# Optimization experiments

Measured on AMD Instinct MI355X. Metric: run time of the kernel, lower is better.

The kernel has to match this reference:

```python
import jax, jax.numpy as jnp
import numpy as np

BETA = 0.25  # commitment_beta


def setup_inputs() -> dict:
    key = jax.random.key(0)
    k1, k2 = jax.random.split(key)
    x = jax.random.normal(k1, (8, 256, 32, 32), dtype=jnp.float32)
    # nn.Embedding weight, uniform(-1/K, 1/K) in the original; use small randn-scaled init
    K, d = 4096, 256
    embed_w = jax.random.uniform(k2, (K, d), dtype=jnp.float32, minval=-1.0 / K, maxval=1.0 / K)
    return {"x": x, "embed_w": embed_w}


def reference(x, embed_w):
    B, C, H, W = x.shape
    N = H * W
    # b c h w -> b (h w) c
    xr = jnp.transpose(x, (0, 2, 3, 1)).reshape(B, N, C)
    flat = xr.reshape(B * N, C)
    dist = (-jnp.sum(flat * flat, axis=1, keepdims=True)
            - jnp.sum(embed_w * embed_w, axis=1)
            + 2.0 * jnp.einsum('nd,kd->nk', flat, embed_w))
    # temp=0.0 -> gumbel_sample degenerates to argmax
    embed_ind = jnp.argmax(dist, axis=-1).reshape(B, N)
    x_q = embed_w[embed_ind]  # [B, N, C] gather
    sg = jax.lax.stop_gradient
    loss = (BETA * jnp.mean((sg(x_q) - xr) ** 2)
            + jnp.mean((x_q - sg(xr)) ** 2))
    # straight-through estimator
    x_q = xr + sg(x_q - xr)
    # b (h w) c -> b c h w
    x_q = jnp.transpose(x_q.reshape(B, H, W, C), (0, 3, 1, 2))
    embed_ind = embed_ind.reshape(B, H, W)
    return (x_q, loss, embed_ind)
```

## Files before the change

### kernel.cpp

```cpp
#include <hip/hip_runtime.h>
#include <stdint.h>


typedef _Float16 f16;
typedef f16 half8 __attribute__((ext_vector_type(8)));
typedef float f32x4 __attribute__((ext_vector_type(4)));

__device__ __forceinline__ unsigned int sortable_f32(float v) {
    unsigned int u = __float_as_uint(v);
    return (u & 0x80000000u) ? ~u : (u | 0x80000000u);
}

__device__ __forceinline__ void gload_lds16(const void* g, void* l) {
    __builtin_amdgcn_global_load_lds(
        (const __attribute__((address_space(1))) unsigned int*)g,
        (__attribute__((address_space(3))) unsigned int*)l, 16, 0, 0);
}

__global__ void vq_prep(const float* __restrict__ x, const float* __restrict__ ew,
                        float* __restrict__ e2, float* __restrict__ negx2,
                        unsigned long long* __restrict__ cand,
                        f16* __restrict__ ehi, f16* __restrict__ elo,
                        f16* __restrict__ xhi, f16* __restrict__ xlo,
                        float* __restrict__ loss_cell) {
    __shared__ float xs[32][132];
    const int u = blockIdx.x, tid = threadIdx.x;
    if (u < 512) {
        const int t = u * 256 + tid;
        const int k = t >> 5, g32 = t & 31;
        const float4 v0 = *(const float4*)(ew + k * 256 + g32 * 8);
        const float4 v1 = *(const float4*)(ew + k * 256 + g32 * 8 + 4);
        const float vf[8] = {v0.x, v0.y, v0.z, v0.w, v1.x, v1.y, v1.z, v1.w};
        half8 h1, h2;
#pragma unroll
        for (int j = 0; j < 8; ++j) {
            const float v = vf[j] * 4096.0f;
            const f16 a = (f16)v;
            const f16 b = (f16)(v - (float)a);
            h1[j] = a; h2[j] = b;
        }
        const int kt = k >> 7, kk = k & 127, ci = g32 >> 2, g = g32 & 3;
        const long off = ((long)((kt * 8 + ci) * 128 + kk)) * 32 + ((g ^ (kk & 3)) * 8);
        *(half8*)(ehi + off) = h1;
        *(half8*)(elo + off) = h2;
    } else if (u < 528) {
        const int k = (u - 512) * 256 + tid;
        const float4* row = (const float4*)(ew + k * 256);
        float s = 0.0f;
#pragma unroll 8
        for (int i = 0; i < 64; ++i) {
            float4 v = row[i];
            s += v.x * v.x + v.y * v.y + v.z * v.z + v.w * v.w;
        }
        e2[k] = s;
    } else if (u < 560) {
        const int z = (u - 528) * 256 + tid;
        cand[z] = 0ull;
        if (z == 0) *loss_cell = 0.0f;
    } else if (u < 592) {
        const int r = (u - 560) * 256 + tid;
        const int b = r >> 10, n = r & 1023;
        const float* px = x + b * 262144 + n;
        float s = 0.0f;
#pragma unroll 8
        for (int c = 0; c < 256; ++c) {
            float v = px[c << 10];
            s += v * v;
        }
        negx2[r] = -s;
    } else {
        const int unit = u - 592;
        const int ci = unit & 7, mt = unit >> 3;
        const int b = mt >> 3, n0 = (mt & 7) * 128, c0 = ci * 32;
#pragma unroll
        for (int it = 0; it < 4; ++it) {
            const int idx = tid + it * 256;
            const int cc = idx >> 5, nn4 = idx & 31;
            float4 v = *(const float4*)(x + b * 262144 + (c0 + cc) * 1024 + n0 + nn4 * 4);
            *(float4*)&xs[cc][nn4 * 4] = v;
        }
        __syncthreads();
#pragma unroll
        for (int it = 0; it < 2; ++it) {
            const int idx = tid + it * 256;
            const int mm = idx & 127, g = idx >> 7;
            half8 h1, h2;
#pragma unroll
            for (int j = 0; j < 8; ++j) {
                const float v = xs[g * 8 + j][mm];
                const f16 a = (f16)v;
                const f16 bb = (f16)(v - (float)a);
                h1[j] = a; h2[j] = bb;
            }
            const long off = ((long)((mt * 8 + ci) * 128 + mm)) * 32 + ((g ^ (mm & 3)) * 8);
            *(half8*)(xhi + off) = h1;
            *(half8*)(xlo + off) = h2;
        }
    }
}

__launch_bounds__(256, 2)
__global__ void vq_gemm(const f16* __restrict__ xhi, const f16* __restrict__ xlo,
                        const f16* __restrict__ ehi, const f16* __restrict__ elo,
                        const float* __restrict__ e2, const float* __restrict__ negx2,
                        unsigned long long* __restrict__ cand) {
    __shared__ __align__(16) f16 lds[8192];
    const int tid = threadIdx.x;
    const int kt = blockIdx.x, mt = blockIdx.y;
    const int lane = tid & 63, wave = tid >> 6;
    const int wm = wave >> 1, wk = wave & 1;
    const int col = lane & 15, quad = lane >> 4;

    f32x4 acc[4][4] = {};

    const f16* gx[2] = { xhi + (size_t)(mt * 8) * 4096, xlo + (size_t)(mt * 8) * 4096 };
    const f16* geh = ehi + (size_t)(kt * 8) * 4096;
    const f16* gel = elo + (size_t)(kt * 8) * 4096;

    int aoff[4], boff[4];
#pragma unroll
    for (int i = 0; i < 4; ++i) {
        const int m = wm * 64 + i * 16 + col;
        aoff[i] = m * 32 + ((quad ^ (m & 3)) * 8);
        const int k = wk * 64 + i * 16 + col;
        boff[i] = k * 32 + ((quad ^ (k & 3)) * 8);
    }

    for (int ci = 0; ci < 8; ++ci) {
        __syncthreads();
        const int go = ci * 4096 + tid * 8;
        char* lb = (char*)lds + wave * 1024;
#pragma unroll
        for (int p = 0; p < 2; ++p) {
            gload_lds16(gx[p] + go,        lb + p * 8192);
            gload_lds16(gx[p] + go + 2048, lb + p * 8192 + 4096);
        }
        half8 bhi4[4], blo4[4];
#pragma unroll
        for (int j = 0; j < 4; ++j) {
            bhi4[j] = *(const half8*)(geh + ci * 4096 + boff[j]);
            blo4[j] = *(const half8*)(gel + ci * 4096 + boff[j]);
        }
        __syncthreads();

        half8 ahi4[4], alo4[4];
#pragma unroll
        for (int i = 0; i < 4; ++i) {
            ahi4[i] = *(const half8*)&lds[aoff[i]];
            alo4[i] = *(const half8*)&lds[4096 + aoff[i]];
        }
#pragma unroll
        for (int i = 0; i < 4; ++i)
#pragma unroll
            for (int j = 0; j < 4; ++j) {
                acc[i][j] = __builtin_amdgcn_mfma_f32_16x16x32_f16(ahi4[i], bhi4[j], acc[i][j], 0, 0, 0);
                acc[i][j] = __builtin_amdgcn_mfma_f32_16x16x32_f16(ahi4[i], blo4[j], acc[i][j], 0, 0, 0);
                acc[i][j] = __builtin_amdgcn_mfma_f32_16x16x32_f16(alo4[i], bhi4[j], acc[i][j], 0, 0, 0);
            }
    }

    const int m0 = mt * 128 + wm * 64, k0 = kt * 128 + wk * 64;
#pragma unroll
    for (int i = 0; i < 4; ++i)
#pragma unroll
        for (int r = 0; r < 4; ++r) {
            const float A = negx2[m0 + i * 16 + quad * 4 + r];
            unsigned long long bk = 0ull;
#pragma unroll
            for (int j = 0; j < 4; ++j) {
                const int k = k0 + j * 16 + col;
                const float t1 = A - e2[k];
                const float dist = t1 + acc[i][j][r] * 0x1p-11f;
                const unsigned long long key =
                    ((unsigned long long)sortable_f32(dist) << 32)
                    | (unsigned long long)(unsigned int)(4095 - k);
                if (key > bk) bk = key;
            }
#pragma unroll
            for (int mask = 1; mask <= 8; mask <<= 1) {
                const unsigned long long o = __shfl_xor(bk, mask, 64);
                if (o > bk) bk = o;
            }
            if (col == i * 4 + r)
                atomicMax(&cand[m0 + i * 16 + quad * 4 + r], bk);
        }
}

__global__ void vq_out(const float* __restrict__ x, const float* __restrict__ ew,
                       const unsigned long long* __restrict__ cand,
                       float* __restrict__ out) {
    __shared__ int sidx[64];
    __shared__ float wsum[4];
    const int tid = threadIdx.x;
    const int r0 = blockIdx.x * 64;
    const int cq0 = blockIdx.y * 64;
    const int b = r0 >> 10, n0 = r0 & 1023;
    if (tid < 64) {
        const int r = r0 + tid;
        const unsigned long long bk = cand[r];
        const int idx = 4095 - (int)(unsigned int)(bk & 0xFFFFFFFFull);
        sidx[tid] = idx;
        if (cq0 == 0) out[2097153 + r] = (float)idx;
    }
    __syncthreads();
    const int nn = tid & 63, cq = tid >> 6;
    const int myidx = sidx[nn];
    float lsum = 0.0f;
#pragma unroll 4
    for (int cb = 0; cb < 16; ++cb) {
        const int c = cq0 + cb * 4 + cq;
        const float ve = ew[myidx * 256 + c];
        const long off = (long)b * 262144 + (c << 10) + n0 + nn;
        const float vx = x[off];
        out[off] = ve;
        const float d = ve - vx;
        lsum += d * d;
    }
#pragma unroll
    for (int o = 32; o > 0; o >>= 1) lsum += __shfl_down(lsum, o, 64);
    if ((tid & 63) == 0) wsum[tid >> 6] = lsum;
    __syncthreads();
    if (tid == 0)
        atomicAdd(&out[2097152],
                  1.25f * ((wsum[0] + wsum[1] + wsum[2] + wsum[3]) / 2097152.0f));
}

extern "C" void kernel_launch(void* const* d_in, const int* in_sizes, int n_in,
                              void* d_out, int out_size, void* d_ws, size_t ws_size,
                              hipStream_t stream) {
    const float* x  = (const float*)d_in[0];
    const float* ew = (const float*)d_in[1];
    float* out = (float*)d_out;

    float* e2 = (float*)d_ws;
    float* negx2 = e2 + 4096;
    unsigned long long* cand = (unsigned long long*)((char*)d_ws + 49152);
    f16* ehi = (f16*)((char*)d_ws + 114688);
    f16* elo = (f16*)((char*)d_ws + 114688 + 2097152);
    f16* xhi = (f16*)out;
    f16* xlo = (f16*)(out + 1048576);

    vq_prep<<<1104, 256, 0, stream>>>(x, ew, e2, negx2, cand,
                                      ehi, elo, xhi, xlo, out + 2097152);
    vq_gemm<<<dim3(32, 64), 256, 0, stream>>>(xhi, xlo, ehi, elo, e2, negx2, cand);
    vq_out<<<dim3(128, 4), 256, 0, stream>>>(x, ew, cand, out);
}
```

Baseline: 153.8 us.

## Switch VQ distance GEMM to 32x32x16 MFMA with per-wave 32-row strips

Restructures the split-fp16 distance GEMM so each wave owns a 32-row strip of x against all 128 codebook columns, using 32x32x16 MFMA instead of 16x16x32 tiles. The accumulator shrinks from 16 f32x4 to 4 f32x16, and launch bounds rise to 3 blocks per SIMD to raise occupancy. B fragments are now loaded from global inside the k-step loop after the barrier, so each wave reads the full codebook tile, which means more global and cache traffic per wave. The argmax epilogue is adapted to the 32x32 output layout with a 5-step shuffle reduction.

```diff
diff --git a/kernel.cpp b/kernel.cpp
--- a/kernel.cpp
+++ b/kernel.cpp
@@ -4,7 +4,7 @@
 
 typedef _Float16 f16;
 typedef f16 half8 __attribute__((ext_vector_type(8)));
-typedef float f32x4 __attribute__((ext_vector_type(4)));
+typedef float f32x16 __attribute__((ext_vector_type(16)));
 
 __device__ __forceinline__ unsigned int sortable_f32(float v) {
     unsigned int u = __float_as_uint(v);
@@ -99,7 +99,7 @@
     }
 }
 
-__launch_bounds__(256, 2)
+__launch_bounds__(256, 3)
 __global__ void vq_gemm(const f16* __restrict__ xhi, const f16* __restrict__ xlo,
                         const f16* __restrict__ ehi, const f16* __restrict__ elo,
                         const float* __restrict__ e2, const float* __restrict__ negx2,
@@ -108,22 +108,22 @@
     const int tid = threadIdx.x;
     const int kt = blockIdx.x, mt = blockIdx.y;
     const int lane = tid & 63, wave = tid >> 6;
-    const int wm = wave >> 1, wk = wave & 1;
-    const int col = lane & 15, quad = lane >> 4;
-
-    f32x4 acc[4][4] = {};
+    const int l31 = lane & 31, hl = lane >> 5;
+
+    f32x16 acc[4] = {};
 
     const f16* gx[2] = { xhi + (size_t)(mt * 8) * 4096, xlo + (size_t)(mt * 8) * 4096 };
     const f16* geh = ehi + (size_t)(kt * 8) * 4096;
     const f16* gel = elo + (size_t)(kt * 8) * 4096;
 
-    int aoff[4], boff[4];
-#pragma unroll
-    for (int i = 0; i < 4; ++i) {
-        const int m = wm * 64 + i * 16 + col;
-        aoff[i] = m * 32 + ((quad ^ (m & 3)) * 8);
-        const int k = wk * 64 + i * 16 + col;
-        boff[i] = k * 32 + ((quad ^ (k & 3)) * 8);
+    const int m = wave * 32 + l31;
+    int aoff[2], boff[4][2];
+#pragma unroll
+    for (int ks = 0; ks < 2; ++ks) {
+        aoff[ks] = m * 32 + (((ks * 2 + hl) ^ (m & 3)) * 8);
+#pragma unroll
+        for (int j = 0; j < 4; ++j)
+            boff[j][ks] = (j * 32 + l31) * 32 + (((ks * 2 + hl) ^ (l31 & 3)) * 8);
     }
 
     for (int ci = 0; ci < 8; ++ci) {
@@ -135,55 +135,52 @@
             gload_lds16(gx[p] + go,        lb + p * 8192);
             gload_lds16(gx[p] + go + 2048, lb + p * 8192 + 4096);
         }
-        half8 bhi4[4], blo4[4];
+        __syncthreads();
+
+#pragma unroll
+        for (int ks = 0; ks < 2; ++ks) {
+            const half8 ah = *(const half8*)&lds[aoff[ks]];
+            const half8 al = *(const half8*)&lds[4096 + aoff[ks]];
+            half8 bh[4], bl[4];
+#pragma unroll
+            for (int j = 0; j < 4; ++j) {
+                bh[j] = *(const half8*)(geh + ci * 4096 + boff[j][ks]);
+                bl[j] = *(const half8*)(gel + ci * 4096 + boff[j][ks]);
+            }
+#pragma unroll
+            for (int j = 0; j < 4; ++j) {
+                acc[j] = __builtin_amdgcn_mfma_f32_32x32x16_f16(ah, bh[j], acc[j], 0, 0, 0);
+                acc[j] = __builtin_amdgcn_mfma_f32_32x32x16_f16(ah, bl[j], acc[j], 0, 0, 0);
+                acc[j] = __builtin_amdgcn_mfma_f32_32x32x16_f16(al, bh[j], acc[j], 0, 0, 0);
+            }
+        }
+    }
+
+    const int m0g = mt * 128 + wave * 32;
+    const int k0g = kt * 128;
+#pragma unroll
+    for (int r = 0; r < 16; ++r) {
+        const int row = (r & 3) + 8 * (r >> 2) + 4 * hl;
+        const int mg = m0g + row;
+        const float A = negx2[mg];
+        unsigned long long bk = 0ull;
 #pragma unroll
         for (int j = 0; j < 4; ++j) {
-            bhi4[j] = *(const half8*)(geh + ci * 4096 + boff[j]);
-            blo4[j] = *(const half8*)(gel + ci * 4096 + boff[j]);
-        }
-        __syncthreads();
-
-        half8 ahi4[4], alo4[4];
-#pragma unroll
-        for (int i = 0; i < 4; ++i) {
-            ahi4[i] = *(const half8*)&lds[aoff[i]];
-            alo4[i] = *(const half8*)&lds[4096 + aoff[i]];
-        }
-#pragma unroll
-        for (int i = 0; i < 4; ++i)
-#pragma unroll
-            for (int j = 0; j < 4; ++j) {
-                acc[i][j] = __builtin_amdgcn_mfma_f32_16x16x32_f16(ahi4[i], bhi4[j], acc[i][j], 0, 0, 0);
-                acc[i][j] = __builtin_amdgcn_mfma_f32_16x16x32_f16(ahi4[i], blo4[j], acc[i][j], 0, 0, 0);
-                acc[i][j] = __builtin_amdgcn_mfma_f32_16x16x32_f16(alo4[i], bhi4[j], acc[i][j], 0, 0, 0);
-            }
-    }
-
-    const int m0 = mt * 128 + wm * 64, k0 = kt * 128 + wk * 64;
-#pragma unroll
-    for (int i = 0; i < 4; ++i)
-#pragma unroll
-        for (int r = 0; r < 4; ++r) {
-            const float A = negx2[m0 + i * 16 + quad * 4 + r];
-            unsigned long long bk = 0ull;
-#pragma unroll
-            for (int j = 0; j < 4; ++j) {
-                const int k = k0 + j * 16 + col;
-                const float t1 = A - e2[k];
-                const float dist = t1 + acc[i][j][r] * 0x1p-11f;
-                const unsigned long long key =
-                    ((unsigned long long)sortable_f32(dist) << 32)
-                    | (unsigned long long)(unsigned int)(4095 - k);
-                if (key > bk) bk = key;
-            }
-#pragma unroll
-            for (int mask = 1; mask <= 8; mask <<= 1) {
-                const unsigned long long o = __shfl_xor(bk, mask, 64);
-                if (o > bk) bk = o;
-            }
-            if (col == i * 4 + r)
-                atomicMax(&cand[m0 + i * 16 + quad * 4 + r], bk);
-        }
+            const int kg = k0g + j * 32 + l31;
+            const float t1 = A - e2[kg];
+            const float dist = t1 + acc[j][r] * 0x1p-11f;
+            const unsigned long long key =
+                ((unsigned long long)sortable_f32(dist) << 32)
+                | (unsigned long long)(unsigned int)(4095 - kg);
+            if (key > bk) bk = key;
+        }
+#pragma unroll
+        for (int mask = 1; mask <= 16; mask <<= 1) {
+            const unsigned long long o = __shfl_xor(bk, mask, 64);
+            if (o > bk) bk = o;
+        }
+        if (l31 == r) atomicMax(&cand[mg], bk);
+    }
 }
 
 __global__ void vq_out(const float* __restrict__ x, const float* __restrict__ ew,
```

New measurement: 166.7 us. 8.4% more time.
